# Kernel optimization log

Measured on AMD Instinct MI355X. Metric: run time of the kernel, lower is better.

The kernel has to match this reference:

```python
import jax, jax.numpy as jnp
import numpy as np

B, S, DIM = 16, 1024, 1024
GAMMA = 0.96875
EPS = 1e-3  # keras GroupNormalization default epsilon


def setup_inputs() -> dict:
    key = jax.random.key(0)
    ks = jax.random.split(key, 4)
    scale = 1.0 / np.sqrt(DIM)
    return {
        "x": jax.random.normal(ks[0], (B, S, DIM), dtype=jnp.float32),
        "Wq": jax.random.normal(ks[1], (DIM, DIM), dtype=jnp.float32) * scale,
        "Wk": jax.random.normal(ks[2], (DIM, DIM), dtype=jnp.float32) * scale,
        "Wv": jax.random.normal(ks[3], (DIM, DIM), dtype=jnp.float32) * scale,
        "gn_scale": jnp.ones((DIM,), dtype=jnp.float32),
        "gn_beta": jnp.zeros((DIM,), dtype=jnp.float32),
    }


def reference(x, Wq, Wk, Wv, gn_scale, gn_beta):
    # Bias-free projections
    Q = x @ Wq  # [B,S,D]
    K = x @ Wk
    V = x @ Wv
    # Full (non-causal) exponential decay matrix D[i,j] = gamma^(i-j)
    idx = jnp.arange(S, dtype=jnp.float32)
    D = GAMMA ** (idx[:, None] - idx[None, :])  # [S,S]
    scores = jnp.einsum("bsd,btd->bst", Q, K) * D  # [B,S,S]
    y = scores @ V  # [B,S,D]
    # GroupNorm with groups == channels: normalize each channel over seq axis
    mean = jnp.mean(y, axis=1, keepdims=True)  # [B,1,D]
    var = jnp.var(y, axis=1, keepdims=True)
    y_hat = (y - mean) * jax.lax.rsqrt(var + EPS)
    return y_hat * gn_scale + gn_beta
```

## Files before the change

### kernel.cpp

```cpp
#include <hip/hip_runtime.h>
#include <cmath>

#define BATCH_ 16
#define SN_ 1024
#define DN_ 1024

constexpr float EPS_ = 1e-3f;

typedef unsigned short ushort;
typedef __attribute__((ext_vector_type(8))) short short8;
typedef __attribute__((ext_vector_type(8))) unsigned short ushort8;
typedef __attribute__((ext_vector_type(16))) float f32x16;

__device__ __forceinline__ ushort f2b(float f) {
    unsigned u = __float_as_uint(f);
    unsigned r = (u + 0x7fffu + ((u >> 16) & 1u)) >> 16;
    return (ushort)r;
}

__device__ __forceinline__ void gload16(const void* g, void* l) {
    __builtin_amdgcn_global_load_lds(
        (const __attribute__((address_space(1))) void*)g,
        (__attribute__((address_space(3))) void*)l, 16, 0, 0);
}

#define SCHED0 __builtin_amdgcn_sched_barrier(0)
#define MFMA32(a, b, c) __builtin_amdgcn_mfma_f32_32x32x16_bf16(a, b, c, 0, 0, 0)

template<int MODE>
__global__ __launch_bounds__(512, 2)
void gemm_bf(const ushort* __restrict__ A0, const ushort* __restrict__ B0,
             void* __restrict__ C0, void* __restrict__ C1, void* __restrict__ C2,
             float* __restrict__ psum, float* __restrict__ psq,
             long sA, long sB, long sBm, long sC, float coef)
{
    __shared__ __align__(16) char lds[131072];

    const int gx = gridDim.x, gy = gridDim.y;
    int lid   = blockIdx.x + gx * (blockIdx.y + gy * blockIdx.z);
    int total = gx * gy * gridDim.z;
    int swz   = (lid & 7) * (total >> 3) + (lid >> 3);
    int bx = swz % gx;
    int rest = swz / gx;
    int by = rest % gy;
    int bz = rest / gy;

    const int m0 = by * 256, n0 = bx * 256;
    const ushort* A  = A0 + (long)bz * sA;
    const ushort* Bp = B0 + (long)bz * sB + (long)(m0 >> 10) * sBm;

    const int t = threadIdx.x;
    const int l = t & 63, w = t >> 6;
    const int wr = w >> 2, wc = w & 3;
    const int ln = l & 31;
    const int kb = l >> 5;
    const int lsh   = ln >> 1;
    const int lodd8 = (ln & 1) * 8;

    const int aOff = wr * 16384 + lsh * 256;
    const int bOff = 32768 + wc * 8192 + lsh * 256;

    const int su = (t & 15) ^ ((t >> 4) & 15);
    const int sc = su & 7;
    const int srow = 2 * (t >> 4) + (su >> 3);
    const ushort* gA = A  + (long)(m0 + srow) * 1024 + sc * 8;
    const ushort* gB = Bp + (long)(n0 + srow) * 1024 + sc * 8;
    char* lA = lds + t * 16;
    char* lB = lds + 32768 + t * 16;

#define STA(h, k0, bo_) gload16(gA + (long)(h) * 65536 + (k0), lA + (bo_) + (h) * 8192)
#define STB(h, k0, bo_) gload16(gB + (long)(h) * 65536 + (k0), lB + (bo_) + (h) * 8192)

    f32x16 acc[4][2] = {};

    STB(0, 0, 0); STB(1, 0, 0); STB(2, 0, 0); STB(3, 0, 0);
    STA(0, 0, 0); STA(1, 0, 0); STA(2, 0, 0); STA(3, 0, 0);
    SCHED0;
    asm volatile("s_waitcnt vmcnt(0)" ::: "memory");
    SCHED0;
    __builtin_amdgcn_s_barrier();
    SCHED0;

    const int kkxor = (w & 1) << 1;

    for (int kt = 0; kt < 16; ++kt) {
        const int bo = (kt & 1) << 16;
        const int bn = bo ^ 65536;
        const int k1 = (kt + 1) << 6;
        const bool st = kt < 15;
        const char* base = lds + bo;

#pragma unroll
        for (int p = 0; p < 4; ++p) {
            const int kk = p ^ kkxor;
            const int sxp = (((kk * 2 + kb) + lodd8) ^ lsh) * 16;
            short8 a0 = *(const short8*)(base + aOff + 0 * 4096 + sxp);
            short8 a1 = *(const short8*)(base + aOff + 1 * 4096 + sxp);
            short8 a2 = *(const short8*)(base + aOff + 2 * 4096 + sxp);
            short8 a3 = *(const short8*)(base + aOff + 3 * 4096 + sxp);
            short8 b0 = *(const short8*)(base + bOff + 0 * 4096 + sxp);
            short8 b1 = *(const short8*)(base + bOff + 1 * 4096 + sxp);
            if (st) {
                if (p == 0) { STB(0, k1, bn); STB(1, k1, bn);
                              STB(2, k1, bn); STB(3, k1, bn); }
                else if (p == 1) { STA(0, k1, bn); STA(1, k1, bn);
                                   STA(2, k1, bn); STA(3, k1, bn); }
            }
            __builtin_amdgcn_s_setprio(1);
            acc[0][0] = MFMA32(a0, b0, acc[0][0]);
            acc[0][1] = MFMA32(a0, b1, acc[0][1]);
            acc[1][0] = MFMA32(a1, b0, acc[1][0]);
            acc[1][1] = MFMA32(a1, b1, acc[1][1]);
            acc[2][0] = MFMA32(a2, b0, acc[2][0]);
            acc[2][1] = MFMA32(a2, b1, acc[2][1]);
            acc[3][0] = MFMA32(a3, b0, acc[3][0]);
            acc[3][1] = MFMA32(a3, b1, acc[3][1]);
            __builtin_amdgcn_s_setprio(0);
            SCHED0;
        }
        asm volatile("s_waitcnt vmcnt(0)" ::: "memory");
        SCHED0;
        __builtin_amdgcn_s_barrier();
        SCHED0;
    }

    if constexpr (MODE == 4) {
        ushort* C = (ushort*)C0 + (long)bz * sC;
#pragma unroll
        for (int mi = 0; mi < 4; ++mi)
#pragma unroll
            for (int reg = 0; reg < 16; ++reg) {
                int row = m0 + wr * 128 + mi * 32 + (reg & 3) + 8 * (reg >> 2) + 4 * kb;
#pragma unroll
                for (int nj = 0; nj < 2; ++nj)
                    C[(long)row * 1024 + n0 + wc * 64 + nj * 32 + ln] =
                        f2b(acc[mi][nj][reg]);
            }
    } else if constexpr (MODE == 5) {
        ushort* C = (ushort*)C0;
        float cs0 = 0.f, cq0 = 0.f, cs1 = 0.f, cq1 = 0.f;
#pragma unroll
        for (int mi = 0; mi < 4; ++mi)
#pragma unroll
            for (int reg = 0; reg < 16; ++reg) {
                float v0 = acc[mi][0][reg], v1 = acc[mi][1][reg];
                cs0 += v0; cq0 += v0 * v0;
                cs1 += v1; cq1 += v1 * v1;
                int row = m0 + wr * 128 + mi * 32 + (reg & 3) + 8 * (reg >> 2) + 4 * kb;
                C[(long)row * 1024 + n0 + wc * 64 + ln]      = f2b(v0);
                C[(long)row * 1024 + n0 + wc * 64 + 32 + ln] = f2b(v1);
            }
        float* S4 = (float*)lds;
        float* Q4 = (float*)(lds + 4096);
        {
            int c0i = wc * 64 + ln, c1i = wc * 64 + 32 + ln, idx = wr * 2 + kb;
            S4[c0i * 4 + idx] = cs0; S4[c1i * 4 + idx] = cs1;
            Q4[c0i * 4 + idx] = cq0; Q4[c1i * 4 + idx] = cq1;
        }
        __syncthreads();
        if (t < 256) {
            float s = S4[t * 4] + S4[t * 4 + 1] + S4[t * 4 + 2] + S4[t * 4 + 3];
            float q = Q4[t * 4] + Q4[t * 4 + 1] + Q4[t * 4 + 2] + Q4[t * 4 + 3];
            psum[(long)by * 1024 + n0 + t] = s;
            psq [(long)by * 1024 + n0 + t] = q;
        }
    } else {
        const int which = n0 >> 10;
        const int nq = n0 & 1023;
        if (which == 0) {
            ushort* C = (ushort*)C0;
#pragma unroll
            for (int mi = 0; mi < 4; ++mi)
#pragma unroll
                for (int reg = 0; reg < 16; ++reg) {
                    int row = m0 + wr * 128 + mi * 32 + (reg & 3) + 8 * (reg >> 2) + 4 * kb;
                    float s = exp2f(coef * (float)(row & 1023));
#pragma unroll
                    for (int nj = 0; nj < 2; ++nj)
                        C[(long)row * 1024 + nq + wc * 64 + nj * 32 + ln] =
                            f2b(acc[mi][nj][reg] * s);
                }
        } else {
            ushort* Tl = (ushort*)lds;
            const int bb = m0 >> 10;
            const int ms = m0 & 1023;
            ushort* Ct = (ushort*)((which == 1) ? C1 : C2) + (long)bb * sC;
            const float cf = (which == 1) ? -coef : 0.0f;
            __syncthreads();
#pragma unroll
            for (int mi = 0; mi < 4; ++mi)
#pragma unroll
                for (int reg = 0; reg < 16; ++reg) {
                    int rm = wr * 128 + mi * 32 + (reg & 3) + 8 * (reg >> 2) + 4 * kb;
                    float s = exp2f(cf * (float)(ms + rm));
#pragma unroll
                    for (int nj = 0; nj < 2; ++nj) {
                        int cn = wc * 64 + nj * 32 + ln;
                        int p  = (rm >> 3) ^ (cn & 31);
                        Tl[cn * 256 + p * 8 + (rm & 7)] = f2b(acc[mi][nj][reg] * s);
                    }
                }
        __syncthreads();
#pragma unroll
            for (int it = 0; it < 16; ++it) {
                int cn = (t >> 5) + it * 16;
                int ch = t & 31;
                int p  = ch ^ (cn & 31);
                ushort8 v = *(const ushort8*)&Tl[cn * 256 + p * 8];
                *(ushort8*)&Ct[(long)(nq + cn) * 1024 + ms + ch * 8] = v;
            }
        }
    }
#undef STA
#undef STB
}

__global__ __launch_bounds__(256)
void conv_x_k(const float* __restrict__ x, ushort* __restrict__ xb)
{
    long i = ((long)blockIdx.x * 256 + threadIdx.x) * 8;
    float4 a = *(const float4*)&x[i];
    float4 b = *(const float4*)&x[i + 4];
    ushort8 v;
    v[0] = f2b(a.x); v[1] = f2b(a.y); v[2] = f2b(a.z); v[3] = f2b(a.w);
    v[4] = f2b(b.x); v[5] = f2b(b.y); v[6] = f2b(b.z); v[7] = f2b(b.w);
    *(ushort8*)&xb[i] = v;
}

__global__ __launch_bounds__(256)
void wt_k(const float* __restrict__ W, ushort* __restrict__ Wt)
{
    __shared__ float Tl[32][33];
    int tx = threadIdx.x & 31, ty = threadIdx.x >> 5;
    int c0 = blockIdx.x * 32, r0 = blockIdx.y * 32;
#pragma unroll
    for (int i = 0; i < 4; i++)
        Tl[ty + 8 * i][tx] = W[(long)(r0 + ty + 8 * i) * 1024 + c0 + tx];
    __syncthreads();
#pragma unroll
    for (int i = 0; i < 4; i++)
        Wt[(long)(c0 + ty + 8 * i) * 1024 + r0 + tx] = f2b(Tl[tx][ty + 8 * i]);
}

__global__ __launch_bounds__(256)
void stats2(const float* __restrict__ psum, const float* __restrict__ psq,
            const float* __restrict__ gsc, const float* __restrict__ gbt,
            float* __restrict__ fs, float* __restrict__ bias)
{
    int d = blockIdx.x * 256 + threadIdx.x;
    int b = blockIdx.y;
    float s = 0.f, q = 0.f;
#pragma unroll
    for (int z = 0; z < 4; z++) {
        long o = ((long)(b * 4 + z) << 10) + d;
        s += psum[o];
        q += psq[o];
    }
    float mean = s * (1.0f / SN_);
    float var  = q * (1.0f / SN_) - mean * mean;
    var = fmaxf(var, 0.0f);
    float rstd = rsqrtf(var + EPS_);
    float f = rstd * gsc[d];
    fs[(long)b * DN_ + d]   = f;
    bias[(long)b * DN_ + d] = gbt[d] - mean * f;
}

__global__ __launch_bounds__(256)
void norm_k(const ushort* __restrict__ yb, const float* __restrict__ fs,
            const float* __restrict__ bias, float* __restrict__ out)
{
    long i = ((long)blockIdx.x * 256 + threadIdx.x) * 8;
    int d = (int)(i & (DN_ - 1));
    int b = (int)(i >> 20);
    ushort8 v = *(const ushort8*)&yb[i];
    long o = (long)b * DN_ + d;
    float4 f0 = *(const float4*)&fs[o];
    float4 f1 = *(const float4*)&fs[o + 4];
    float4 b0 = *(const float4*)&bias[o];
    float4 b1 = *(const float4*)&bias[o + 4];
    float4 o0, o1;
    o0.x = __uint_as_float((unsigned)v[0] << 16) * f0.x + b0.x;
    o0.y = __uint_as_float((unsigned)v[1] << 16) * f0.y + b0.y;
    o0.z = __uint_as_float((unsigned)v[2] << 16) * f0.z + b0.z;
    o0.w = __uint_as_float((unsigned)v[3] << 16) * f0.w + b0.w;
    o1.x = __uint_as_float((unsigned)v[4] << 16) * f1.x + b1.x;
    o1.y = __uint_as_float((unsigned)v[5] << 16) * f1.y + b1.y;
    o1.z = __uint_as_float((unsigned)v[6] << 16) * f1.z + b1.z;
    o1.w = __uint_as_float((unsigned)v[7] << 16) * f1.w + b1.w;
    *(float4*)&out[i]     = o0;
    *(float4*)&out[i + 4] = o1;
}

extern "C" void kernel_launch(void* const* d_in, const int* in_sizes, int n_in,
                              void* d_out, int out_size, void* d_ws, size_t ws_size,
                              hipStream_t stream)
{
    const float* x   = (const float*)d_in[0];
    const float* Wq  = (const float*)d_in[1];
    const float* Wk  = (const float*)d_in[2];
    const float* Wv  = (const float*)d_in[3];
    const float* gsc = (const float*)d_in[4];
    const float* gbt = (const float*)d_in[5];
    float* out = (float*)d_out;

    const long SD = (long)SN_ * DN_;
    const long DD = (long)DN_ * DN_;
    const size_t MB32 = (size_t)SD * BATCH_ * sizeof(ushort);

    char* ws = (char*)d_ws;
    ushort* xb  = (ushort*)(ws);
    ushort* Qp  = (ushort*)(ws + 1 * MB32);
    ushort* Kt  = (ushort*)(ws + 2 * MB32);
    ushort* Vt  = (ushort*)(ws + 3 * MB32);
    ushort* Mt  = (ushort*)(ws + 4 * MB32);
    ushort* Wct = (ushort*)(ws + 5 * MB32);
    float*  psum = (float*)(ws + 5 * MB32 + (6u << 20));
    float*  psq  = (float*)(ws + 5 * MB32 + (6u << 20) + (1u << 18));
    float*  fs   = (float*)(ws + 5 * MB32 + (6u << 20) + (2u << 18));
    float*  bias = (float*)(ws + 5 * MB32 + (6u << 20) + (2u << 18) + (1u << 16));
    ushort* yb  = xb;

    const float lgf = (float)log2(0.96875);

    dim3 blk512(512);
    dim3 blk(256);
    dim3 gproj(12, 64);
    dim3 gmt(4, 4, 16);
    dim3 gy(4, 64);

    conv_x_k<<<dim3(8192), blk, 0, stream>>>(x, xb);
    wt_k<<<dim3(32, 32), blk, 0, stream>>>(Wq, Wct);
    wt_k<<<dim3(32, 32), blk, 0, stream>>>(Wk, Wct + 1024 * 1024);
    wt_k<<<dim3(32, 32), blk, 0, stream>>>(Wv, Wct + 2 * 1024 * 1024);

    gemm_bf<6><<<gproj, blk512, 0, stream>>>(xb, Wct, Qp, Kt, Vt,
                                             nullptr, nullptr,
                                             0, 0, 0, SD, lgf);
    gemm_bf<4><<<gmt, blk512, 0, stream>>>(Vt, Kt, Mt, nullptr, nullptr,
                                           nullptr, nullptr,
                                           SD, SD, 0, DD, 0.0f);
    gemm_bf<5><<<gy, blk512, 0, stream>>>(Qp, Mt, yb, nullptr, nullptr,
                                          psum, psq,
                                          0, 0, DD, 0, 0.0f);

    stats2<<<dim3(4, 16), blk, 0, stream>>>(psum, psq, gsc, gbt, fs, bias);
    norm_k<<<dim3(8192), blk, 0, stream>>>(yb, fs, bias, out);
}
```

Baseline: 236.1 us.

## Use 4-wave blocks with 128x128 per-wave tiles in bf16 GEMMs

Moves the GEMM kernel from 8 waves per 256x256 block (each wave computing a 128x64 tile) to 4 waves per block, each computing a 128x128 tile with a 4x4 MFMA accumulator grid. This raises the MFMA-to-LDS-read ratio per wave and halves the number of waves contending for LDS. The cost is twice the accumulator registers per wave and fewer waves per CU to hide latency, since the 128 KB LDS already limits each CU to one block. Each thread now issues 8 global-to-LDS loads per operand, and the epilogues are adjusted to match. The per-wave k-order xor staggering and the inner sched barrier are also removed.

```diff
diff --git a/kernel.cpp b/kernel.cpp
--- a/kernel.cpp
+++ b/kernel.cpp
@@ -28,7 +28,7 @@
 #define MFMA32(a, b, c) __builtin_amdgcn_mfma_f32_32x32x16_bf16(a, b, c, 0, 0, 0)
 
 template<int MODE>
-__global__ __launch_bounds__(512, 2)
+__global__ __launch_bounds__(256, 1)
 void gemm_bf(const ushort* __restrict__ A0, const ushort* __restrict__ B0,
              void* __restrict__ C0, void* __restrict__ C1, void* __restrict__ C2,
              float* __restrict__ psum, float* __restrict__ psq,
@@ -51,16 +51,16 @@
 
     const int t = threadIdx.x;
     const int l = t & 63, w = t >> 6;
-    const int wr = w >> 2, wc = w & 3;
+    const int wr = w >> 1, wc = w & 1;
     const int ln = l & 31;
     const int kb = l >> 5;
     const int lsh   = ln >> 1;
     const int lodd8 = (ln & 1) * 8;
 
     const int aOff = wr * 16384 + lsh * 256;
-    const int bOff = 32768 + wc * 8192 + lsh * 256;
-
-    const int su = (t & 15) ^ ((t >> 4) & 15);
+    const int bOff = 32768 + wc * 16384 + lsh * 256;
+
+    const int su = (t & 15) ^ (t >> 4);
     const int sc = su & 7;
     const int srow = 2 * (t >> 4) + (su >> 3);
     const ushort* gA = A  + (long)(m0 + srow) * 1024 + sc * 8;
@@ -68,55 +68,62 @@
     char* lA = lds + t * 16;
     char* lB = lds + 32768 + t * 16;
 
-#define STA(h, k0, bo_) gload16(gA + (long)(h) * 65536 + (k0), lA + (bo_) + (h) * 8192)
-#define STB(h, k0, bo_) gload16(gB + (long)(h) * 65536 + (k0), lB + (bo_) + (h) * 8192)
-
-    f32x16 acc[4][2] = {};
-
-    STB(0, 0, 0); STB(1, 0, 0); STB(2, 0, 0); STB(3, 0, 0);
-    STA(0, 0, 0); STA(1, 0, 0); STA(2, 0, 0); STA(3, 0, 0);
+#define STA(h, k0, bo_) gload16(gA + (long)(h) * 32768 + (k0), lA + (bo_) + (h) * 4096)
+#define STB(h, k0, bo_) gload16(gB + (long)(h) * 32768 + (k0), lB + (bo_) + (h) * 4096)
+#define STA8(k0, bo_) do { STA(0,k0,bo_); STA(1,k0,bo_); STA(2,k0,bo_); STA(3,k0,bo_); \
+                           STA(4,k0,bo_); STA(5,k0,bo_); STA(6,k0,bo_); STA(7,k0,bo_); } while (0)
+#define STB8(k0, bo_) do { STB(0,k0,bo_); STB(1,k0,bo_); STB(2,k0,bo_); STB(3,k0,bo_); \
+                           STB(4,k0,bo_); STB(5,k0,bo_); STB(6,k0,bo_); STB(7,k0,bo_); } while (0)
+
+    f32x16 acc[4][4] = {};
+
+    STB8(0, 0);
+    STA8(0, 0);
     SCHED0;
     asm volatile("s_waitcnt vmcnt(0)" ::: "memory");
     SCHED0;
     __builtin_amdgcn_s_barrier();
     SCHED0;
 
-    const int kkxor = (w & 1) << 1;
-
     for (int kt = 0; kt < 16; ++kt) {
-        const int bo = (kt & 1) << 16;
-        const int bn = bo ^ 65536;
+        const char* base = lds + ((kt & 1) << 16);
+        const int bn = ((kt + 1) & 1) << 16;
         const int k1 = (kt + 1) << 6;
         const bool st = kt < 15;
-        const char* base = lds + bo;
-
-#pragma unroll
-        for (int p = 0; p < 4; ++p) {
-            const int kk = p ^ kkxor;
-            const int sxp = (((kk * 2 + kb) + lodd8) ^ lsh) * 16;
-            short8 a0 = *(const short8*)(base + aOff + 0 * 4096 + sxp);
-            short8 a1 = *(const short8*)(base + aOff + 1 * 4096 + sxp);
-            short8 a2 = *(const short8*)(base + aOff + 2 * 4096 + sxp);
-            short8 a3 = *(const short8*)(base + aOff + 3 * 4096 + sxp);
-            short8 b0 = *(const short8*)(base + bOff + 0 * 4096 + sxp);
-            short8 b1 = *(const short8*)(base + bOff + 1 * 4096 + sxp);
+
+#pragma unroll
+        for (int ks = 0; ks < 4; ++ks) {
+            const int sxp = (((ks * 2 + kb) + lodd8) ^ lsh) * 16;
+            short8 fa0 = *(const short8*)(base + aOff + 0 * 4096 + sxp);
+            short8 fa1 = *(const short8*)(base + aOff + 1 * 4096 + sxp);
+            short8 fa2 = *(const short8*)(base + aOff + 2 * 4096 + sxp);
+            short8 fa3 = *(const short8*)(base + aOff + 3 * 4096 + sxp);
+            short8 fb0 = *(const short8*)(base + bOff + 0 * 4096 + sxp);
+            short8 fb1 = *(const short8*)(base + bOff + 1 * 4096 + sxp);
+            short8 fb2 = *(const short8*)(base + bOff + 2 * 4096 + sxp);
+            short8 fb3 = *(const short8*)(base + bOff + 3 * 4096 + sxp);
             if (st) {
-                if (p == 0) { STB(0, k1, bn); STB(1, k1, bn);
-                              STB(2, k1, bn); STB(3, k1, bn); }
-                else if (p == 1) { STA(0, k1, bn); STA(1, k1, bn);
-                                   STA(2, k1, bn); STA(3, k1, bn); }
+                if (ks == 0) STB8(k1, bn);
+                else if (ks == 1) STA8(k1, bn);
             }
             __builtin_amdgcn_s_setprio(1);
-            acc[0][0] = MFMA32(a0, b0, acc[0][0]);
-            acc[0][1] = MFMA32(a0, b1, acc[0][1]);
-            acc[1][0] = MFMA32(a1, b0, acc[1][0]);
-            acc[1][1] = MFMA32(a1, b1, acc[1][1]);
-            acc[2][0] = MFMA32(a2, b0, acc[2][0]);
-            acc[2][1] = MFMA32(a2, b1, acc[2][1]);
-            acc[3][0] = MFMA32(a3, b0, acc[3][0]);
-            acc[3][1] = MFMA32(a3, b1, acc[3][1]);
+            acc[0][0] = MFMA32(fa0, fb0, acc[0][0]);
+            acc[0][1] = MFMA32(fa0, fb1, acc[0][1]);
+            acc[0][2] = MFMA32(fa0, fb2, acc[0][2]);
+            acc[0][3] = MFMA32(fa0, fb3, acc[0][3]);
+            acc[1][0] = MFMA32(fa1, fb0, acc[1][0]);
+            acc[1][1] = MFMA32(fa1, fb1, acc[1][1]);
+            acc[1][2] = MFMA32(fa1, fb2, acc[1][2]);
+            acc[1][3] = MFMA32(fa1, fb3, acc[1][3]);
+            acc[2][0] = MFMA32(fa2, fb0, acc[2][0]);
+            acc[2][1] = MFMA32(fa2, fb1, acc[2][1]);
+            acc[2][2] = MFMA32(fa2, fb2, acc[2][2]);
+            acc[2][3] = MFMA32(fa2, fb3, acc[2][3]);
+            acc[3][0] = MFMA32(fa3, fb0, acc[3][0]);
+            acc[3][1] = MFMA32(fa3, fb1, acc[3][1]);
+            acc[3][2] = MFMA32(fa3, fb2, acc[3][2]);
+            acc[3][3] = MFMA32(fa3, fb3, acc[3][3]);
             __builtin_amdgcn_s_setprio(0);
-            SCHED0;
         }
         asm volatile("s_waitcnt vmcnt(0)" ::: "memory");
         SCHED0;
@@ -132,33 +139,38 @@
             for (int reg = 0; reg < 16; ++reg) {
                 int row = m0 + wr * 128 + mi * 32 + (reg & 3) + 8 * (reg >> 2) + 4 * kb;
 #pragma unroll
-                for (int nj = 0; nj < 2; ++nj)
-                    C[(long)row * 1024 + n0 + wc * 64 + nj * 32 + ln] =
+                for (int nj = 0; nj < 4; ++nj)
+                    C[(long)row * 1024 + n0 + wc * 128 + nj * 32 + ln] =
                         f2b(acc[mi][nj][reg]);
             }
     } else if constexpr (MODE == 5) {
         ushort* C = (ushort*)C0;
-        float cs0 = 0.f, cq0 = 0.f, cs1 = 0.f, cq1 = 0.f;
+        float cs[4] = {0.f, 0.f, 0.f, 0.f}, cq[4] = {0.f, 0.f, 0.f, 0.f};
 #pragma unroll
         for (int mi = 0; mi < 4; ++mi)
 #pragma unroll
             for (int reg = 0; reg < 16; ++reg) {
-                float v0 = acc[mi][0][reg], v1 = acc[mi][1][reg];
-                cs0 += v0; cq0 += v0 * v0;
-                cs1 += v1; cq1 += v1 * v1;
                 int row = m0 + wr * 128 + mi * 32 + (reg & 3) + 8 * (reg >> 2) + 4 * kb;
-                C[(long)row * 1024 + n0 + wc * 64 + ln]      = f2b(v0);
-                C[(long)row * 1024 + n0 + wc * 64 + 32 + ln] = f2b(v1);
+#pragma unroll
+                for (int nj = 0; nj < 4; ++nj) {
+                    float v = acc[mi][nj][reg];
+                    cs[nj] += v; cq[nj] += v * v;
+                    C[(long)row * 1024 + n0 + wc * 128 + nj * 32 + ln] = f2b(v);
+                }
             }
         float* S4 = (float*)lds;
         float* Q4 = (float*)(lds + 4096);
         {
-            int c0i = wc * 64 + ln, c1i = wc * 64 + 32 + ln, idx = wr * 2 + kb;
-            S4[c0i * 4 + idx] = cs0; S4[c1i * 4 + idx] = cs1;
-            Q4[c0i * 4 + idx] = cq0; Q4[c1i * 4 + idx] = cq1;
+            int idx = wr * 2 + kb;
+#pragma unroll
+            for (int nj = 0; nj < 4; ++nj) {
+                int ci = wc * 128 + nj * 32 + ln;
+                S4[ci * 4 + idx] = cs[nj];
+                Q4[ci * 4 + idx] = cq[nj];
+            }
         }
         __syncthreads();
-        if (t < 256) {
+        {
             float s = S4[t * 4] + S4[t * 4 + 1] + S4[t * 4 + 2] + S4[t * 4 + 3];
             float q = Q4[t * 4] + Q4[t * 4 + 1] + Q4[t * 4 + 2] + Q4[t * 4 + 3];
             psum[(long)by * 1024 + n0 + t] = s;
@@ -176,8 +188,8 @@
                     int row = m0 + wr * 128 + mi * 32 + (reg & 3) + 8 * (reg >> 2) + 4 * kb;
                     float s = exp2f(coef * (float)(row & 1023));
 #pragma unroll
-                    for (int nj = 0; nj < 2; ++nj)
-                        C[(long)row * 1024 + nq + wc * 64 + nj * 32 + ln] =
+                    for (int nj = 0; nj < 4; ++nj)
+                        C[(long)row * 1024 + nq + wc * 128 + nj * 32 + ln] =
                             f2b(acc[mi][nj][reg] * s);
                 }
         } else {
@@ -194,16 +206,16 @@
                     int rm = wr * 128 + mi * 32 + (reg & 3) + 8 * (reg >> 2) + 4 * kb;
                     float s = exp2f(cf * (float)(ms + rm));
 #pragma unroll
-                    for (int nj = 0; nj < 2; ++nj) {
-                        int cn = wc * 64 + nj * 32 + ln;
+                    for (int nj = 0; nj < 4; ++nj) {
+                        int cn = wc * 128 + nj * 32 + ln;
                         int p  = (rm >> 3) ^ (cn & 31);
                         Tl[cn * 256 + p * 8 + (rm & 7)] = f2b(acc[mi][nj][reg] * s);
                     }
                 }
-        __syncthreads();
-#pragma unroll
-            for (int it = 0; it < 16; ++it) {
-                int cn = (t >> 5) + it * 16;
+            __syncthreads();
+#pragma unroll
+            for (int it = 0; it < 32; ++it) {
+                int cn = it * 8 + (t >> 5);
                 int ch = t & 31;
                 int p  = ch ^ (cn & 31);
                 ushort8 v = *(const ushort8*)&Tl[cn * 256 + p * 8];
@@ -213,6 +225,8 @@
     }
 #undef STA
 #undef STB
+#undef STA8
+#undef STB8
 }
 
 __global__ __launch_bounds__(256)
@@ -322,7 +336,6 @@
 
     const float lgf = (float)log2(0.96875);
 
-    dim3 blk512(512);
     dim3 blk(256);
     dim3 gproj(12, 64);
     dim3 gmt(4, 4, 16);
@@ -333,15 +346,15 @@
     wt_k<<<dim3(32, 32), blk, 0, stream>>>(Wk, Wct + 1024 * 1024);
     wt_k<<<dim3(32, 32), blk, 0, stream>>>(Wv, Wct + 2 * 1024 * 1024);
 
-    gemm_bf<6><<<gproj, blk512, 0, stream>>>(xb, Wct, Qp, Kt, Vt,
-                                             nullptr, nullptr,
-                                             0, 0, 0, SD, lgf);
-    gemm_bf<4><<<gmt, blk512, 0, stream>>>(Vt, Kt, Mt, nullptr, nullptr,
-                                           nullptr, nullptr,
-                                           SD, SD, 0, DD, 0.0f);
-    gemm_bf<5><<<gy, blk512, 0, stream>>>(Qp, Mt, yb, nullptr, nullptr,
-                                          psum, psq,
-                                          0, 0, DD, 0, 0.0f);
+    gemm_bf<6><<<gproj, blk, 0, stream>>>(xb, Wct, Qp, Kt, Vt,
+                                          nullptr, nullptr,
+                                          0, 0, 0, SD, lgf);
+    gemm_bf<4><<<gmt, blk, 0, stream>>>(Vt, Kt, Mt, nullptr, nullptr,
+                                        nullptr, nullptr,
+                                        SD, SD, 0, DD, 0.0f);
+    gemm_bf<5><<<gy, blk, 0, stream>>>(Qp, Mt, yb, nullptr, nullptr,
+                                       psum, psq,
+                                       0, 0, DD, 0, 0.0f);
 
     stats2<<<dim3(4, 16), blk, 0, stream>>>(psum, psq, gsc, gbt, fs, bias);
     norm_k<<<dim3(8192), blk, 0, stream>>>(yb, fs, bias, out);
```

Measured after the change: 241.6 us. 1.02x slower.

## Switch GEMM to 16x16x32 MFMA with four-phase LDS/global pipelined main loop

Applied to the files above, without the earlier changes.

Replaces the 32x32x16 bf16 MFMA tiling with 16x16x32 MFMAs over 8x4 accumulator fragments per wave. The main loop becomes a four-phase schedule that interleaves fragment reads, half-tile global-to-LDS staging for the next and next-next k-steps, and MFMA quadrants separated by barriers. The goal is to overlap memory traffic with matrix math more finely and hide LDS latency. Epilogue index math is adapted to the new fragment layout, and the column statistics now reduce over 8 partials. The extra barriers and the changed LDS access pattern could add synchronization overhead or bank conflicts.

```diff
diff --git a/kernel.cpp b/kernel.cpp
--- a/kernel.cpp
+++ b/kernel.cpp
@@ -10,7 +10,7 @@
 typedef unsigned short ushort;
 typedef __attribute__((ext_vector_type(8))) short short8;
 typedef __attribute__((ext_vector_type(8))) unsigned short ushort8;
-typedef __attribute__((ext_vector_type(16))) float f32x16;
+typedef __attribute__((ext_vector_type(4))) float f32x4;
 
 __device__ __forceinline__ ushort f2b(float f) {
     unsigned u = __float_as_uint(f);
@@ -25,11 +25,13 @@
 }
 
 #define SCHED0 __builtin_amdgcn_sched_barrier(0)
-#define MFMA32(a, b, c) __builtin_amdgcn_mfma_f32_32x32x16_bf16(a, b, c, 0, 0, 0)
+#define BAR do { __builtin_amdgcn_s_barrier(); asm volatile("" ::: "memory"); } while (0)
+#define WLG0 do { asm volatile("s_waitcnt lgkmcnt(0)" ::: "memory"); SCHED0; } while (0)
+#define MFMA16(a, b, c) __builtin_amdgcn_mfma_f32_16x16x32_bf16(a, b, c, 0, 0, 0)
 
 template<int MODE>
 __global__ __launch_bounds__(512, 2)
-void gemm_bf(const ushort* __restrict__ A0, const ushort* __restrict__ B0,
+void gemm_bf(const ushort* __restrict__ A0p, const ushort* __restrict__ B0p,
              void* __restrict__ C0, void* __restrict__ C1, void* __restrict__ C2,
              float* __restrict__ psum, float* __restrict__ psq,
              long sA, long sB, long sBm, long sC, float coef)
@@ -46,19 +48,31 @@
     int bz = rest / gy;
 
     const int m0 = by * 256, n0 = bx * 256;
-    const ushort* A  = A0 + (long)bz * sA;
-    const ushort* Bp = B0 + (long)bz * sB + (long)(m0 >> 10) * sBm;
+    const ushort* A  = A0p + (long)bz * sA;
+    const ushort* Bp = B0p + (long)bz * sB + (long)(m0 >> 10) * sBm;
 
     const int t = threadIdx.x;
     const int l = t & 63, w = t >> 6;
     const int wr = w >> 2, wc = w & 3;
-    const int ln = l & 31;
-    const int kb = l >> 5;
-    const int lsh   = ln >> 1;
-    const int lodd8 = (ln & 1) * 8;
-
-    const int aOff = wr * 16384 + lsh * 256;
-    const int bOff = 32768 + wc * 8192 + lsh * 256;
+    const int lc  = l & 15;
+    const int chi = l >> 4;
+    const int par8 = (l & 1) * 8;
+
+    int baseA[8], xorA[8], baseB[4], xorB[4];
+#pragma unroll
+    for (int mf = 0; mf < 8; ++mf) {
+        int r = wr * 128 + mf * 16 + lc, g = r >> 1;
+        baseA[mf] = (g >> 6) * 16384 + (g & 63) * 256;
+        xorA[mf]  = g & 15;
+    }
+#pragma unroll
+    for (int nf = 0; nf < 4; ++nf) {
+        int r = wc * 64 + nf * 16 + lc, g = r >> 1;
+        baseB[nf] = 32768 + (g >> 6) * 16384 + (g & 63) * 256;
+        xorB[nf]  = g & 15;
+    }
+    const int ck0 = chi | par8;
+    const int ck1 = (chi + 4) | par8;
 
     const int su = (t & 15) ^ ((t >> 4) & 15);
     const int sc = su & 7;
@@ -68,99 +82,120 @@
     char* lA = lds + t * 16;
     char* lB = lds + 32768 + t * 16;
 
-#define STA(h, k0, bo_) gload16(gA + (long)(h) * 65536 + (k0), lA + (bo_) + (h) * 8192)
-#define STB(h, k0, bo_) gload16(gB + (long)(h) * 65536 + (k0), lB + (bo_) + (h) * 8192)
-
-    f32x16 acc[4][2] = {};
-
-    STB(0, 0, 0); STB(1, 0, 0); STB(2, 0, 0); STB(3, 0, 0);
-    STA(0, 0, 0); STA(1, 0, 0); STA(2, 0, 0); STA(3, 0, 0);
+#define STAGE_A(h, k0, bo_) do { \
+    gload16(gA + (long)(h) * 131072 + (k0), lA + (bo_) + (h) * 16384); \
+    gload16(gA + (long)(h) * 131072 + 65536 + (k0), lA + (bo_) + (h) * 16384 + 8192); } while (0)
+#define STAGE_B(h, k0, bo_) do { \
+    gload16(gB + (long)(h) * 131072 + (k0), lB + (bo_) + (h) * 16384); \
+    gload16(gB + (long)(h) * 131072 + 65536 + (k0), lB + (bo_) + (h) * 16384 + 8192); } while (0)
+
+#define RDA(S, mh) do { \
+    _Pragma("unroll") for (int mf_ = 0; mf_ < 4; ++mf_) { \
+        S[mf_][0] = *(const short8*)(lds + bo + baseA[(mh)*4+mf_] + ((ck0 ^ xorA[(mh)*4+mf_]) << 4)); \
+        S[mf_][1] = *(const short8*)(lds + bo + baseA[(mh)*4+mf_] + ((ck1 ^ xorA[(mh)*4+mf_]) << 4)); } } while (0)
+#define RDB(S, nh) do { \
+    _Pragma("unroll") for (int nf_ = 0; nf_ < 2; ++nf_) { \
+        S[nf_][0] = *(const short8*)(lds + bo + baseB[(nh)*2+nf_] + ((ck0 ^ xorB[(nh)*2+nf_]) << 4)); \
+        S[nf_][1] = *(const short8*)(lds + bo + baseB[(nh)*2+nf_] + ((ck1 ^ xorB[(nh)*2+nf_]) << 4)); } } while (0)
+
+#define MPH(mh, nh, SA_, SB_) do { \
+    __builtin_amdgcn_s_setprio(1); \
+    _Pragma("unroll") for (int ks_ = 0; ks_ < 2; ++ks_) \
+    _Pragma("unroll") for (int mf_ = 0; mf_ < 4; ++mf_) \
+    _Pragma("unroll") for (int nf_ = 0; nf_ < 2; ++nf_) \
+        acc[(mh)*4+mf_][(nh)*2+nf_] = MFMA16(SA_[mf_][ks_], SB_[nf_][ks_], \
+                                             acc[(mh)*4+mf_][(nh)*2+nf_]); \
+    __builtin_amdgcn_s_setprio(0); } while (0)
+
+    f32x4 acc[8][4] = {};
+    short8 Af0[4][2], Af1[4][2], Bf0[2][2], Bf1[2][2];
+
+    STAGE_A(0, 0, 0); STAGE_A(1, 0, 0); STAGE_B(0, 0, 0); STAGE_B(1, 0, 0);
+    STAGE_A(0, 64, 65536);
     SCHED0;
-    asm volatile("s_waitcnt vmcnt(0)" ::: "memory");
-    SCHED0;
-    __builtin_amdgcn_s_barrier();
-    SCHED0;
-
-    const int kkxor = (w & 1) << 1;
+    asm volatile("s_waitcnt vmcnt(2)" ::: "memory");
+    BAR;
 
     for (int kt = 0; kt < 16; ++kt) {
         const int bo = (kt & 1) << 16;
         const int bn = bo ^ 65536;
         const int k1 = (kt + 1) << 6;
-        const bool st = kt < 15;
-        const char* base = lds + bo;
-
-#pragma unroll
-        for (int p = 0; p < 4; ++p) {
-            const int kk = p ^ kkxor;
-            const int sxp = (((kk * 2 + kb) + lodd8) ^ lsh) * 16;
-            short8 a0 = *(const short8*)(base + aOff + 0 * 4096 + sxp);
-            short8 a1 = *(const short8*)(base + aOff + 1 * 4096 + sxp);
-            short8 a2 = *(const short8*)(base + aOff + 2 * 4096 + sxp);
-            short8 a3 = *(const short8*)(base + aOff + 3 * 4096 + sxp);
-            short8 b0 = *(const short8*)(base + bOff + 0 * 4096 + sxp);
-            short8 b1 = *(const short8*)(base + bOff + 1 * 4096 + sxp);
-            if (st) {
-                if (p == 0) { STB(0, k1, bn); STB(1, k1, bn);
-                              STB(2, k1, bn); STB(3, k1, bn); }
-                else if (p == 1) { STA(0, k1, bn); STA(1, k1, bn);
-                                   STA(2, k1, bn); STA(3, k1, bn); }
-            }
-            __builtin_amdgcn_s_setprio(1);
-            acc[0][0] = MFMA32(a0, b0, acc[0][0]);
-            acc[0][1] = MFMA32(a0, b1, acc[0][1]);
-            acc[1][0] = MFMA32(a1, b0, acc[1][0]);
-            acc[1][1] = MFMA32(a1, b1, acc[1][1]);
-            acc[2][0] = MFMA32(a2, b0, acc[2][0]);
-            acc[2][1] = MFMA32(a2, b1, acc[2][1]);
-            acc[3][0] = MFMA32(a3, b0, acc[3][0]);
-            acc[3][1] = MFMA32(a3, b1, acc[3][1]);
-            __builtin_amdgcn_s_setprio(0);
+        const int k2 = (kt + 2) << 6;
+
+        RDA(Af0, 0); RDB(Bf0, 0);
+        if (kt < 15) STAGE_A(1, k1, bn);
+        asm volatile("s_waitcnt lgkmcnt(8)" ::: "memory");
+        BAR; WLG0;
+        MPH(0, 0, Af0, Bf0);
+        SCHED0; BAR;
+
+        RDB(Bf1, 1);
+        if (kt < 15) STAGE_B(0, k1, bn);
+        BAR; WLG0;
+        MPH(0, 1, Af0, Bf1);
+        SCHED0; BAR;
+
+        RDA(Af1, 1);
+        if (kt < 15) STAGE_B(1, k1, bn);
+        BAR; WLG0;
+        MPH(1, 0, Af1, Bf0);
+        SCHED0; BAR;
+
+        if (kt < 14) {
+            STAGE_A(0, k2, bo);
             SCHED0;
+            asm volatile("s_waitcnt vmcnt(2)" ::: "memory");
+        } else {
+            asm volatile("s_waitcnt vmcnt(0)" ::: "memory");
         }
-        asm volatile("s_waitcnt vmcnt(0)" ::: "memory");
-        SCHED0;
-        __builtin_amdgcn_s_barrier();
-        SCHED0;
+        BAR;
+        MPH(1, 1, Af1, Bf1);
+        SCHED0; BAR;
     }
 
     if constexpr (MODE == 4) {
         ushort* C = (ushort*)C0 + (long)bz * sC;
 #pragma unroll
-        for (int mi = 0; mi < 4; ++mi)
-#pragma unroll
-            for (int reg = 0; reg < 16; ++reg) {
-                int row = m0 + wr * 128 + mi * 32 + (reg & 3) + 8 * (reg >> 2) + 4 * kb;
-#pragma unroll
-                for (int nj = 0; nj < 2; ++nj)
-                    C[(long)row * 1024 + n0 + wc * 64 + nj * 32 + ln] =
-                        f2b(acc[mi][nj][reg]);
+        for (int mf = 0; mf < 8; ++mf)
+#pragma unroll
+            for (int q = 0; q < 4; ++q) {
+                int row = m0 + wr * 128 + mf * 16 + chi * 4 + q;
+#pragma unroll
+                for (int nf = 0; nf < 4; ++nf)
+                    C[(long)row * 1024 + n0 + wc * 64 + nf * 16 + lc] =
+                        f2b(acc[mf][nf][q]);
             }
     } else if constexpr (MODE == 5) {
         ushort* C = (ushort*)C0;
-        float cs0 = 0.f, cq0 = 0.f, cs1 = 0.f, cq1 = 0.f;
-#pragma unroll
-        for (int mi = 0; mi < 4; ++mi)
-#pragma unroll
-            for (int reg = 0; reg < 16; ++reg) {
-                float v0 = acc[mi][0][reg], v1 = acc[mi][1][reg];
-                cs0 += v0; cq0 += v0 * v0;
-                cs1 += v1; cq1 += v1 * v1;
-                int row = m0 + wr * 128 + mi * 32 + (reg & 3) + 8 * (reg >> 2) + 4 * kb;
-                C[(long)row * 1024 + n0 + wc * 64 + ln]      = f2b(v0);
-                C[(long)row * 1024 + n0 + wc * 64 + 32 + ln] = f2b(v1);
+        float cs[4] = {0.f, 0.f, 0.f, 0.f}, cq[4] = {0.f, 0.f, 0.f, 0.f};
+#pragma unroll
+        for (int mf = 0; mf < 8; ++mf)
+#pragma unroll
+            for (int q = 0; q < 4; ++q) {
+                int row = m0 + wr * 128 + mf * 16 + chi * 4 + q;
+#pragma unroll
+                for (int nf = 0; nf < 4; ++nf) {
+                    float v = acc[mf][nf][q];
+                    cs[nf] += v; cq[nf] += v * v;
+                    C[(long)row * 1024 + n0 + wc * 64 + nf * 16 + lc] = f2b(v);
+                }
             }
         float* S4 = (float*)lds;
-        float* Q4 = (float*)(lds + 4096);
+        float* Q4 = (float*)(lds + 8192);
         {
-            int c0i = wc * 64 + ln, c1i = wc * 64 + 32 + ln, idx = wr * 2 + kb;
-            S4[c0i * 4 + idx] = cs0; S4[c1i * 4 + idx] = cs1;
-            Q4[c0i * 4 + idx] = cq0; Q4[c1i * 4 + idx] = cq1;
+            int idx = wr * 4 + chi;
+#pragma unroll
+            for (int nf = 0; nf < 4; ++nf) {
+                int ci = wc * 64 + nf * 16 + lc;
+                S4[ci * 8 + idx] = cs[nf];
+                Q4[ci * 8 + idx] = cq[nf];
+            }
         }
         __syncthreads();
         if (t < 256) {
-            float s = S4[t * 4] + S4[t * 4 + 1] + S4[t * 4 + 2] + S4[t * 4 + 3];
-            float q = Q4[t * 4] + Q4[t * 4 + 1] + Q4[t * 4 + 2] + Q4[t * 4 + 3];
+            float s = 0.f, q = 0.f;
+#pragma unroll
+            for (int z = 0; z < 8; ++z) { s += S4[t * 8 + z]; q += Q4[t * 8 + z]; }
             psum[(long)by * 1024 + n0 + t] = s;
             psq [(long)by * 1024 + n0 + t] = q;
         }
@@ -170,15 +205,15 @@
         if (which == 0) {
             ushort* C = (ushort*)C0;
 #pragma unroll
-            for (int mi = 0; mi < 4; ++mi)
-#pragma unroll
-                for (int reg = 0; reg < 16; ++reg) {
-                    int row = m0 + wr * 128 + mi * 32 + (reg & 3) + 8 * (reg >> 2) + 4 * kb;
+            for (int mf = 0; mf < 8; ++mf)
+#pragma unroll
+                for (int q = 0; q < 4; ++q) {
+                    int row = m0 + wr * 128 + mf * 16 + chi * 4 + q;
                     float s = exp2f(coef * (float)(row & 1023));
 #pragma unroll
-                    for (int nj = 0; nj < 2; ++nj)
-                        C[(long)row * 1024 + nq + wc * 64 + nj * 32 + ln] =
-                            f2b(acc[mi][nj][reg] * s);
+                    for (int nf = 0; nf < 4; ++nf)
+                        C[(long)row * 1024 + nq + wc * 64 + nf * 16 + lc] =
+                            f2b(acc[mf][nf][q] * s);
                 }
         } else {
             ushort* Tl = (ushort*)lds;
@@ -188,19 +223,19 @@
             const float cf = (which == 1) ? -coef : 0.0f;
             __syncthreads();
 #pragma unroll
-            for (int mi = 0; mi < 4; ++mi)
-#pragma unroll
-                for (int reg = 0; reg < 16; ++reg) {
-                    int rm = wr * 128 + mi * 32 + (reg & 3) + 8 * (reg >> 2) + 4 * kb;
+            for (int mf = 0; mf < 8; ++mf)
+#pragma unroll
+                for (int q = 0; q < 4; ++q) {
+                    int rm = wr * 128 + mf * 16 + chi * 4 + q;
                     float s = exp2f(cf * (float)(ms + rm));
 #pragma unroll
-                    for (int nj = 0; nj < 2; ++nj) {
-                        int cn = wc * 64 + nj * 32 + ln;
+                    for (int nf = 0; nf < 4; ++nf) {
+                        int cn = wc * 64 + nf * 16 + lc;
                         int p  = (rm >> 3) ^ (cn & 31);
-                        Tl[cn * 256 + p * 8 + (rm & 7)] = f2b(acc[mi][nj][reg] * s);
+                        Tl[cn * 256 + p * 8 + (rm & 7)] = f2b(acc[mf][nf][q] * s);
                     }
                 }
-        __syncthreads();
+            __syncthreads();
 #pragma unroll
             for (int it = 0; it < 16; ++it) {
                 int cn = (t >> 5) + it * 16;
@@ -211,8 +246,11 @@
             }
         }
     }
-#undef STA
-#undef STB
+#undef STAGE_A
+#undef STAGE_B
+#undef RDA
+#undef RDB
+#undef MPH
 }
 
 __global__ __launch_bounds__(256)
```

Measured after the change: 228.7 us. -3.2%, faster.
